# Optimization experiments

Measured on AMD Instinct MI355X. Metric: run time of the kernel, lower is better.

## Reference

```python
import jax, jax.numpy as jnp
import numpy as np

T, N = 64, 1048576  # bitstream length, number of parallel unary channels


def setup_inputs() -> dict:
    key = jax.random.key(0)
    kbits = jax.random.fold_in(key, 1)
    # unary bitstream: each bit is 0 or 1 (Bernoulli(0.5)); stored as float,
    # matching bstype=torch.float output / int8-on-{0,1} internal math exactly.
    bits = (jax.random.uniform(kbits, (T, N)) < 0.5).astype(jnp.float32)
    trace0 = jnp.zeros((N,), jnp.float32)  # JKFF state, torch inits zeros(1)
    return {"input": bits, "trace0": trace0}


def reference(input, trace0):
    # UnarySqrt with emit=False, mode='unipolar', jk_trace=True.
    # Per torch forward (python precedence: `1 - trace & input` == (1-trace)&input):
    #   output = ((1 - trace) & input) + trace
    #   trace' = JKFF(J=output, K=1)  ->  Q' = J & ~Q = output & (1 - trace)
    # On {0,1} bits, AND == multiply; the add is disjoint so stays exact.
    def step(trace, x):
        out = (1.0 - trace) * x + trace
        trace_next = out * (1.0 - trace)
        return trace_next, out

    _, outs = jax.lax.scan(step, trace0, input)  # outs: [T, N]
    return outs
```

## Files before the change

kernel.cpp:

```cpp
#include <hip/hip_runtime.h>
#include <stdint.h>


typedef float v4f __attribute__((ext_vector_type(4)));

__global__ __launch_bounds__(1024) void UnarySqrt_kernel(
    const v4f* __restrict__ in,
    const v4f* __restrict__ trace0,
    v4f* __restrict__ out,
    int stride)
{
    const int idx = blockIdx.x * blockDim.x + threadIdx.x;
    if (idx >= stride) return;

    v4f tr = trace0[idx];
    v4f x  = __builtin_nontemporal_load(&in[idx]);

    #pragma unroll 8
    for (int t = 0; t < 64; ++t) {
        v4f xn;
        if (t + 1 < 64) {
            xn = __builtin_nontemporal_load(
                &in[(size_t)(t + 1) * (size_t)stride + (size_t)idx]);
        }
        v4f p = x * (1.0f - tr);
        v4f o = tr + p;
        out[(size_t)t * (size_t)stride + (size_t)idx] = o;
        tr = p;
        x = xn;
    }
}

__global__ __launch_bounds__(256) void UnarySqrt_generic(
    const v4f* __restrict__ in, const v4f* __restrict__ trace0,
    v4f* __restrict__ out, int stride, int T)
{
    int idx = blockIdx.x * blockDim.x + threadIdx.x;
    if (idx >= stride) return;
    v4f tr = trace0[idx];
    for (int t = 0; t < T; ++t) {
        v4f x = in[(size_t)t * stride + idx];
        v4f p = x * (1.0f - tr);
        out[(size_t)t * stride + idx] = tr + p;
        tr = p;
    }
}

extern "C" void kernel_launch(void* const* d_in, const int* in_sizes, int n_in,
                              void* d_out, int out_size, void* d_ws, size_t ws_size,
                              hipStream_t stream) {
    const float* bits   = (const float*)d_in[0];
    const float* trace0 = (const float*)d_in[1];

    int N = in_sizes[1];
    int T = in_sizes[0] / N;
    int stride = N / 4;

    if (T == 64 && (stride % 1024) == 0) {
        int grid = stride / 1024;
        UnarySqrt_kernel<<<grid, 1024, 0, stream>>>(
            (const v4f*)bits, (const v4f*)trace0, (v4f*)d_out, stride);
    } else {
        int block = 256;
        int grid = (stride + block - 1) / block;
        UnarySqrt_generic<<<grid, block, 0, stream>>>(
            (const v4f*)bits, (const v4f*)trace0, (v4f*)d_out, stride, T);
    }
}
```

Before: 435.5 us.

## Split scan into bit-packing pass and float expansion pass via workspace

Replaces the single fused scan kernel with two kernels. The first reads the input bitstream, runs the JK recurrence with integer bit logic and packs the 64 output bits per channel into two 32-bit words in workspace. The second expands those bits into float outputs. Separating the read-heavy and write-heavy phases may change how DRAM traffic is scheduled, but it adds a second launch and a small extra workspace round trip, and it assumes the inputs are exactly 0 or 1.

```diff
diff --git a/kernel.cpp b/kernel.cpp
--- a/kernel.cpp
+++ b/kernel.cpp
@@ -3,12 +3,84 @@
 
 
 typedef float v4f __attribute__((ext_vector_type(4)));
+typedef uint32_t v4u __attribute__((ext_vector_type(4)));
+
+__global__ __launch_bounds__(1024) void UnarySqrt_pack(
+    const v4f* __restrict__ in,
+    const v4f* __restrict__ trace0,
+    v4u* __restrict__ ws_lo,
+    v4u* __restrict__ ws_hi,
+    int stride)
+{
+    const int idx = blockIdx.x * blockDim.x + threadIdx.x;
+    if (idx >= stride) return;
+
+    v4f t0 = trace0[idx];
+    uint32_t tr[4];
+    #pragma unroll
+    for (int j = 0; j < 4; ++j) tr[j] = (t0[j] != 0.0f) ? 1u : 0u;
+
+    v4u lo = {0u, 0u, 0u, 0u};
+    #pragma unroll 8
+    for (int t = 0; t < 32; ++t) {
+        v4f x = __builtin_nontemporal_load(
+            &in[(size_t)t * (size_t)stride + (size_t)idx]);
+        #pragma unroll
+        for (int j = 0; j < 4; ++j) {
+            uint32_t xb = (x[j] != 0.0f) ? 1u : 0u;
+            lo[j] |= (xb | tr[j]) << t;
+            tr[j] = xb & (tr[j] ^ 1u);
+        }
+    }
+    v4u hi = {0u, 0u, 0u, 0u};
+    #pragma unroll 8
+    for (int t = 32; t < 64; ++t) {
+        v4f x = __builtin_nontemporal_load(
+            &in[(size_t)t * (size_t)stride + (size_t)idx]);
+        #pragma unroll
+        for (int j = 0; j < 4; ++j) {
+            uint32_t xb = (x[j] != 0.0f) ? 1u : 0u;
+            hi[j] |= (xb | tr[j]) << (t - 32);
+            tr[j] = xb & (tr[j] ^ 1u);
+        }
+    }
+    ws_lo[idx] = lo;
+    ws_hi[idx] = hi;
+}
+
+__global__ __launch_bounds__(1024) void UnarySqrt_expand(
+    const v4u* __restrict__ ws_lo,
+    const v4u* __restrict__ ws_hi,
+    v4f* __restrict__ out,
+    int stride)
+{
+    const int idx = blockIdx.x * blockDim.x + threadIdx.x;
+    if (idx >= stride) return;
+
+    v4u lo = ws_lo[idx];
+    v4u hi = ws_hi[idx];
+
+    #pragma unroll 8
+    for (int t = 0; t < 32; ++t) {
+        v4f o;
+        #pragma unroll
+        for (int j = 0; j < 4; ++j)
+            o[j] = ((lo[j] >> t) & 1u) ? 1.0f : 0.0f;
+        out[(size_t)t * (size_t)stride + (size_t)idx] = o;
+    }
+    #pragma unroll 8
+    for (int t = 32; t < 64; ++t) {
+        v4f o;
+        #pragma unroll
+        for (int j = 0; j < 4; ++j)
+            o[j] = ((hi[j] >> (t - 32)) & 1u) ? 1.0f : 0.0f;
+        out[(size_t)t * (size_t)stride + (size_t)idx] = o;
+    }
+}
 
 __global__ __launch_bounds__(1024) void UnarySqrt_kernel(
-    const v4f* __restrict__ in,
-    const v4f* __restrict__ trace0,
-    v4f* __restrict__ out,
-    int stride)
+    const v4f* __restrict__ in, const v4f* __restrict__ trace0,
+    v4f* __restrict__ out, int stride)
 {
     const int idx = blockIdx.x * blockDim.x + threadIdx.x;
     if (idx >= stride) return;
@@ -56,7 +128,17 @@
     int T = in_sizes[0] / N;
     int stride = N / 4;
 
-    if (T == 64 && (stride % 1024) == 0) {
+    size_t ws_needed = (size_t)stride * 2 * sizeof(v4u);
+
+    if (T == 64 && (stride % 1024) == 0 && d_ws && ws_size >= ws_needed) {
+        int grid = stride / 1024;
+        v4u* ws_lo = (v4u*)d_ws;
+        v4u* ws_hi = ws_lo + stride;
+        UnarySqrt_pack<<<grid, 1024, 0, stream>>>(
+            (const v4f*)bits, (const v4f*)trace0, ws_lo, ws_hi, stride);
+        UnarySqrt_expand<<<grid, 1024, 0, stream>>>(
+            ws_lo, ws_hi, (v4f*)d_out, stride);
+    } else if (T == 64 && (stride % 1024) == 0) {
         int grid = stride / 1024;
         UnarySqrt_kernel<<<grid, 1024, 0, stream>>>(
             (const v4f*)bits, (const v4f*)trace0, (v4f*)d_out, stride);
```

Result: faster. 425.0 us (-2.4%).

## Split the time recurrence into parallel chunks composed as bit-level affine maps

Applied to the files above, without the earlier changes.

Adds a kernel that splits the 64-step recurrence into 4 chunks of 16, each handled by its own thread. Each thread computes its chunk's output bits for both possible starting traces and the chunk's overall trace map, written as a GF(2) affine map packed into bits. Chunk maps are passed through shared memory, and each thread composes its predecessors' maps to find its true starting trace, then picks the matching output bits. The aim is four times more threads and more loads in flight, easing the per-thread serial latency chain, at the cost of a block barrier, extra bit logic, and relying on inputs being exactly 0 or 1.

```diff
diff --git a/kernel.cpp b/kernel.cpp
--- a/kernel.cpp
+++ b/kernel.cpp
@@ -4,11 +4,76 @@
 
 typedef float v4f __attribute__((ext_vector_type(4)));
 
-__global__ __launch_bounds__(1024) void UnarySqrt_kernel(
+#define SPLIT 4
+#define CHUNK 16
+#define COLS  64
+
+__global__ __launch_bounds__(256) void UnarySqrt_tsplit(
     const v4f* __restrict__ in,
     const v4f* __restrict__ trace0,
     v4f* __restrict__ out,
     int stride)
+{
+    __shared__ uint32_t ab[SPLIT][COLS];
+
+    const int c = threadIdx.x & (COLS - 1);
+    const int s = threadIdx.x >> 6;
+    const int idx = blockIdx.x * COLS + c;
+    const int tbase = s * CHUNK;
+
+    uint32_t a = 0u, b = 0xFu;
+    uint32_t o0[4] = {0u, 0u, 0u, 0u};
+    uint32_t o1[4] = {0u, 0u, 0u, 0u};
+    #pragma unroll 4
+    for (int u = 0; u < CHUNK; ++u) {
+        v4f x = in[(size_t)(tbase + u) * (size_t)stride + (size_t)idx];
+        #pragma unroll
+        for (int j = 0; j < 4; ++j) {
+            uint32_t xb = (x[j] != 0.0f) ? 1u : 0u;
+            uint32_t aj = (a >> j) & 1u;
+            uint32_t bj = (b >> j) & 1u;
+            o0[j] |= (xb | aj) << u;
+            o1[j] |= (xb | (aj ^ bj)) << u;
+            uint32_t an = xb & (aj ^ 1u);
+            uint32_t bn = xb & bj;
+            a = (a & ~(1u << j)) | (an << j);
+            b = (b & ~(1u << j)) | (bn << j);
+        }
+    }
+    ab[s][c] = a | (b << 4);
+    __syncthreads();
+
+    v4f t0v = trace0[idx];
+    uint32_t T[4];
+    #pragma unroll
+    for (int j = 0; j < 4; ++j) T[j] = (t0v[j] != 0.0f) ? 1u : 0u;
+    for (int ss = 0; ss < s; ++ss) {
+        uint32_t w = ab[ss][c];
+        #pragma unroll
+        for (int j = 0; j < 4; ++j) {
+            uint32_t A = (w >> j) & 1u;
+            uint32_t B = (w >> (4 + j)) & 1u;
+            T[j] = A ^ (B & T[j]);
+        }
+    }
+
+    uint32_t sel[4];
+    #pragma unroll
+    for (int j = 0; j < 4; ++j) sel[j] = T[j] ? o1[j] : o0[j];
+
+    #pragma unroll 4
+    for (int u = 0; u < CHUNK; ++u) {
+        v4f o;
+        #pragma unroll
+        for (int j = 0; j < 4; ++j)
+            o[j] = (float)((sel[j] >> u) & 1u);
+        out[(size_t)(tbase + u) * (size_t)stride + (size_t)idx] = o;
+    }
+}
+
+__global__ __launch_bounds__(1024) void UnarySqrt_kernel(
+    const v4f* __restrict__ in, const v4f* __restrict__ trace0,
+    v4f* __restrict__ out, int stride)
 {
     const int idx = blockIdx.x * blockDim.x + threadIdx.x;
     if (idx >= stride) return;
@@ -56,7 +121,11 @@
     int T = in_sizes[0] / N;
     int stride = N / 4;
 
-    if (T == 64 && (stride % 1024) == 0) {
+    if (T == 64 && (stride % COLS) == 0) {
+        int grid = stride / COLS;
+        UnarySqrt_tsplit<<<grid, COLS * SPLIT, 0, stream>>>(
+            (const v4f*)bits, (const v4f*)trace0, (v4f*)d_out, stride);
+    } else if (T == 64 && (stride % 1024) == 0) {
         int grid = stride / 1024;
         UnarySqrt_kernel<<<grid, 1024, 0, stream>>>(
             (const v4f*)bits, (const v4f*)trace0, (v4f*)d_out, stride);
```

Result: no change. 443.5 us (+1.9%).

## Replace per-channel float recurrence with bit-packed parallel prefix scan pipeline

Applied to the files above, without the earlier changes.

Splits the computation into three kernels. The first packs the float bitstream into 64-bit ballot masks in a workspace. The second transposes each mask with wave shuffles, evaluates the trace recurrence as a log-step bitwise prefix scan over the 64 timesteps, and transposes back. The third expands the result bits into floats. The aim is to drop the serial 64-step dependency chain per channel and expose more parallelism across waves, at the cost of two extra launches, workspace traffic and scattered 8-byte writes. The path only runs when a large enough workspace is provided.

```diff
diff --git a/kernel.cpp b/kernel.cpp
--- a/kernel.cpp
+++ b/kernel.cpp
@@ -3,12 +3,117 @@
 
 
 typedef float v4f __attribute__((ext_vector_type(4)));
+typedef unsigned long long u64;
+
+
+__global__ __launch_bounds__(256) void UnarySqrt_packA(
+    const v4f* __restrict__ in, u64* __restrict__ P, int nseg)
+{
+    const int l = threadIdx.x & 63;
+    const int wid = threadIdx.x >> 6;
+    const int stride_v4 = nseg * 64;
+    const int ntask = 64 * nseg;
+    const int nwave = gridDim.x * 4;
+
+    for (int task = blockIdx.x * 4 + wid; task < ntask; task += nwave) {
+        const int t = task / nseg;
+        const int s = task - t * nseg;
+        v4f x = in[(size_t)t * stride_v4 + s * 64 + l];
+        u64 b0 = __ballot(x[0] != 0.0f);
+        u64 b1 = __ballot(x[1] != 0.0f);
+        u64 b2 = __ballot(x[2] != 0.0f);
+        u64 b3 = __ballot(x[3] != 0.0f);
+        if (l < 4) {
+            u64 w = (l == 0) ? b0 : (l == 1) ? b1 : (l == 2) ? b2 : b3;
+            P[((size_t)s * 4 + l) * 64 + t] = w;
+        }
+    }
+}
+
+__device__ __forceinline__ u64 xpose64(u64 w, const int lane)
+{
+    u64 t;
+    t = __shfl_xor(w, 32);
+    w = (lane & 32) ? ((w & 0xFFFFFFFF00000000ull) | ((t & 0xFFFFFFFF00000000ull) >> 32))
+                    : ((w & 0x00000000FFFFFFFFull) | ((t & 0x00000000FFFFFFFFull) << 32));
+    t = __shfl_xor(w, 16);
+    w = (lane & 16) ? ((w & 0xFFFF0000FFFF0000ull) | ((t & 0xFFFF0000FFFF0000ull) >> 16))
+                    : ((w & 0x0000FFFF0000FFFFull) | ((t & 0x0000FFFF0000FFFFull) << 16));
+    t = __shfl_xor(w, 8);
+    w = (lane & 8)  ? ((w & 0xFF00FF00FF00FF00ull) | ((t & 0xFF00FF00FF00FF00ull) >> 8))
+                    : ((w & 0x00FF00FF00FF00FFull) | ((t & 0x00FF00FF00FF00FFull) << 8));
+    t = __shfl_xor(w, 4);
+    w = (lane & 4)  ? ((w & 0xF0F0F0F0F0F0F0F0ull) | ((t & 0xF0F0F0F0F0F0F0F0ull) >> 4))
+                    : ((w & 0x0F0F0F0F0F0F0F0Full) | ((t & 0x0F0F0F0F0F0F0F0Full) << 4));
+    t = __shfl_xor(w, 2);
+    w = (lane & 2)  ? ((w & 0xCCCCCCCCCCCCCCCCull) | ((t & 0xCCCCCCCCCCCCCCCCull) >> 2))
+                    : ((w & 0x3333333333333333ull) | ((t & 0x3333333333333333ull) << 2));
+    t = __shfl_xor(w, 1);
+    w = (lane & 1)  ? ((w & 0xAAAAAAAAAAAAAAAAull) | ((t & 0xAAAAAAAAAAAAAAAAull) >> 1))
+                    : ((w & 0x5555555555555555ull) | ((t & 0x5555555555555555ull) << 1));
+    return w;
+}
+
+__device__ __forceinline__ u64 scan_sel(u64 X, u64 T0mask)
+{
+    u64 A = X << 1;
+    u64 B = A | 1ull;
+    #pragma unroll
+    for (int i = 0; i < 6; ++i) {
+        const int d = 1 << i;
+        u64 Ash = A << d;
+        u64 Bsh = (B << d) | ((1ull << d) - 1ull);
+        A ^= (B & Ash);
+        B &= Bsh;
+    }
+    return X | (A ^ (B & T0mask));
+}
+
+__global__ __launch_bounds__(256) void UnarySqrt_scanB(
+    const u64* __restrict__ P, const v4f* __restrict__ trace0,
+    u64* __restrict__ Q, int nseg)
+{
+    const int lane = threadIdx.x & 63;
+    const int k = threadIdx.x >> 6;
+
+    for (int s = blockIdx.x; s < nseg; s += gridDim.x) {
+        u64 w = P[((size_t)s * 4 + k) * 64 + lane];
+        w = xpose64(w, lane);
+        v4f t0 = trace0[s * 64 + lane];
+        u64 T0mask = (t0[k] != 0.0f) ? ~0ull : 0ull;
+        w = scan_sel(w, T0mask);
+        w = xpose64(w, lane);
+        Q[((size_t)s * 4 + k) * 64 + lane] = w;
+    }
+}
+
+__global__ __launch_bounds__(256) void UnarySqrt_expandC(
+    const u64* __restrict__ Q, v4f* __restrict__ out, int nseg)
+{
+    const int nsc = nseg >> 2;
+    const int ntask = 64 * nsc;
+    const int l = threadIdx.x & 63;
+    const int sl = threadIdx.x >> 6;
+    const int stride_v4 = nseg * 64;
+
+    for (int bid = blockIdx.x; bid < ntask; bid += gridDim.x) {
+        const int t = bid / nsc;
+        const int sc = bid - t * nsc;
+        const int s = sc * 4 + sl;
+        const u64* q = &Q[(size_t)s * 256 + t];
+        u64 w0 = q[0], w1 = q[64], w2 = q[128], w3 = q[192];
+        v4f o;
+        o[0] = (float)((w0 >> l) & 1ull);
+        o[1] = (float)((w1 >> l) & 1ull);
+        o[2] = (float)((w2 >> l) & 1ull);
+        o[3] = (float)((w3 >> l) & 1ull);
+        out[(size_t)t * stride_v4 + (size_t)sc * 256 + threadIdx.x] = o;
+    }
+}
 
 __global__ __launch_bounds__(1024) void UnarySqrt_kernel(
-    const v4f* __restrict__ in,
-    const v4f* __restrict__ trace0,
-    v4f* __restrict__ out,
-    int stride)
+    const v4f* __restrict__ in, const v4f* __restrict__ trace0,
+    v4f* __restrict__ out, int stride)
 {
     const int idx = blockIdx.x * blockDim.x + threadIdx.x;
     if (idx >= stride) return;
@@ -56,7 +161,21 @@
     int T = in_sizes[0] / N;
     int stride = N / 4;
 
-    if (T == 64 && (stride % 1024) == 0) {
+    int nseg = N / 256;
+    size_t ws_needed = (size_t)nseg * 4096;
+
+    if (T == 64 && (N % 1024) == 0 && d_ws && ws_size >= ws_needed) {
+        u64* P = (u64*)d_ws;
+        u64* Q = P + (size_t)nseg * 256;
+
+        UnarySqrt_packA<<<2048, 256, 0, stream>>>(
+            (const v4f*)bits, P, nseg);
+        int bgrid = nseg < 4096 ? nseg : 4096;
+        UnarySqrt_scanB<<<bgrid, 256, 0, stream>>>(
+            P, (const v4f*)trace0, Q, nseg);
+        UnarySqrt_expandC<<<16384, 256, 0, stream>>>(
+            Q, (v4f*)d_out, nseg);
+    } else if (T == 64 && (stride % 1024) == 0) {
         int grid = stride / 1024;
         UnarySqrt_kernel<<<grid, 1024, 0, stream>>>(
             (const v4f*)bits, (const v4f*)trace0, (v4f*)d_out, stride);
```

Measured after the change: 457.9 us. +5.2%, slower.
